# Optimization experiments

Measured on AMD Instinct MI355X. Metric: run time of the kernel, lower is better.

Reference implementation:

```python
import jax, jax.numpy as jnp
import numpy as np

EMB = 64
D = 2 * EMB          # 128, feature dim of R / hidden of attention MLP
B, L = 128, 4096     # batch, sequence length
N_ITER = 50          # bisection iterations (entmax_bisect default)


def entmax_bisect(X, alpha, n_iter=N_ITER):
    """alpha-entmax via bisection over the last axis. X: [B, L], alpha: [B, 1] (>1)."""
    am1 = alpha - 1.0
    Xs = X * am1
    d = X.shape[-1]
    inv = 1.0 / am1
    max_val = jnp.max(Xs, axis=-1, keepdims=True)
    tau_lo0 = max_val - 1.0                       # gp(1, alpha) = 1
    tau_hi = max_val - (1.0 / d) ** am1           # gp(1/d, alpha)

    def p(tau):
        return jnp.clip(Xs - tau, 0.0, None) ** inv

    f_lo = jnp.sum(p(tau_lo0), axis=-1, keepdims=True) - 1.0

    def body(i, carry):
        tau_lo, dm, _ = carry
        dm = dm * 0.5
        tau_m = tau_lo + dm
        f_m = jnp.sum(p(tau_m), axis=-1, keepdims=True) - 1.0
        tau_lo = jnp.where(f_m * f_lo >= 0, tau_m, tau_lo)
        return (tau_lo, dm, tau_m)

    _, _, tau_m = jax.lax.fori_loop(0, n_iter, body, (tau_lo0, tau_hi - tau_lo0, tau_lo0))
    p_m = p(tau_m)
    return p_m / jnp.sum(p_m, axis=-1, keepdims=True)  # ensure_sum_one


def setup_inputs() -> dict:
    key = jax.random.key(0)
    ks = jax.random.split(key, 9)
    s = 1.0 / np.sqrt(D)
    R = jax.random.normal(ks[0], (B, L, D), dtype=jnp.float32)
    alpha = 1.25 + 0.5 * jax.random.uniform(ks[1], (B, 1), dtype=jnp.float32)  # in (1.25, 1.75)
    target = jax.random.normal(ks[2], (B, 1, D), dtype=jnp.float32)
    Wr1 = s * jax.random.normal(ks[3], (D, D), dtype=jnp.float32)      # Linear(2E, 2E), no bias
    Wr2 = s * jax.random.normal(ks[4], (D, EMB), dtype=jnp.float32)    # Linear(E, 2E) (shape-fixed), no bias
    Wr3 = s * jax.random.normal(ks[5], (1, D), dtype=jnp.float32)      # Linear(2E, 1), no bias
    bias_r = s * jax.random.normal(ks[6], (D,), dtype=jnp.float32)
    Wf_w = s * jax.random.normal(ks[7], (EMB, D), dtype=jnp.float32)   # Linear(2E, E)
    Wf_b = s * jax.random.normal(ks[8], (EMB,), dtype=jnp.float32)
    return {"R": R, "alpha": alpha, "target": target, "Wr1": Wr1, "Wr2": Wr2,
            "Wr3": Wr3, "bias_r": bias_r, "Wf_w": Wf_w, "Wf_b": Wf_b}


def reference(R, alpha, target, Wr1, Wr2, Wr3, bias_r, Wf_w, Wf_b):
    # q = Wf(target): [B, 1, E]
    q = jnp.einsum('btd,ed->bte', target, Wf_w) + Wf_b
    # additive attention score: Wr3 @ relu(Wr1 k + Wr2 q + b): [B, L]
    h = jax.nn.relu(jnp.einsum('bld,ed->ble', R, Wr1)
                    + jnp.einsum('bte,de->btd', q, Wr2)
                    + bias_r)
    scores = jnp.einsum('bld,d->bl', h, Wr3[0])
    # entmax sparsification over the sequence axis
    a = entmax_bisect(scores, alpha)
    # weighted sum of v = R: [B, D]
    res = jnp.einsum('bl,bld->bd', a, R)
    res = jax.nn.selu(res)
    res = res / jnp.linalg.norm(res, axis=-1, keepdims=True)
    return res
```

## Files before the change

### kernel.cpp

```cpp
#include <hip/hip_runtime.h>
#include <hip/hip_bf16.h>

#define B_ 128
#define L_ 4096
#define D_ 128
#define E_ 64

typedef __attribute__((ext_vector_type(8))) short short8;
typedef __attribute__((ext_vector_type(4))) float floatx4;

static __device__ __forceinline__ unsigned short f2bf(float x) {
  __hip_bfloat16 h = __float2bfloat16(x);
  union { __hip_bfloat16 h; unsigned short u; } c; c.h = h; return c.u;
}
static __device__ __forceinline__ float bf2f(unsigned short u) {
  union { unsigned short u; __hip_bfloat16 h; } c; c.u = u; return __bfloat162float(c.h);
}

__global__ __launch_bounds__(256) void prep(
    const float* __restrict__ Wr1, unsigned short* __restrict__ hi,
    unsigned short* __restrict__ lo, const float* __restrict__ target,
    const float* __restrict__ Wr2, const float* __restrict__ bias_r,
    const float* __restrict__ Wf_w, const float* __restrict__ Wf_b,
    float* __restrict__ cvec) {
  if (blockIdx.x < 64) {
    int t = blockIdx.x * 256 + threadIdx.x;
    int j = t & 7, lane = (t >> 3) & 63, ks = (t >> 9) & 3, nt = t >> 11;
    int e = nt * 16 + (lane & 15);
    int d = ks * 32 + (lane >> 4) * 8 + j;
    float x = Wr1[e * D_ + d];
    unsigned short h = f2bf(x);
    hi[t] = h;
    lo[t] = f2bf(x - bf2f(h));
  } else {
    const int sub = threadIdx.x >> 7;
    const int t = threadIdx.x & 127;
    const int b = (blockIdx.x - 64) * 2 + sub;
    __shared__ float tg[2][D_];
    __shared__ float q[2][E_];
    tg[sub][t] = target[b * D_ + t];
    __syncthreads();
    if (t < E_) {
      float s = Wf_b[t];
      #pragma unroll 8
      for (int d = 0; d < D_; ++d) s += tg[sub][d] * Wf_w[t * D_ + d];
      q[sub][t] = s;
    }
    __syncthreads();
    float s = bias_r[t];
    #pragma unroll 8
    for (int e = 0; e < E_; ++e) s += q[sub][e] * Wr2[t * E_ + e];
    cvec[b * D_ + t] = s;
  }
}

__global__ __launch_bounds__(256, 2) void pass_b(
    const float* __restrict__ R, const unsigned short* __restrict__ Whi,
    const unsigned short* __restrict__ Wlo, const float* __restrict__ cvec,
    const float* __restrict__ Wr3, float* __restrict__ scores) {
  __shared__ __align__(16) unsigned short sAhi[16384];
  __shared__ __align__(16) unsigned short sAlo[16384];
  const int b = blockIdx.x >> 5;
  const int lt = blockIdx.x & 31;
  const int t = threadIdx.x;
  const int wave = t >> 6, lane = t & 63;
  const int col = lane & 15, quad = lane >> 4;

  const float* Rbase = R + ((size_t)b * L_ + (size_t)lt * 128) * D_;
  #pragma unroll
  for (int i = 0; i < 8; ++i) {
    const int mt = wave * 2 + (i >> 2);
    const int ks = i & 3;
    const int row = mt * 16 + (lane & 15);
    const int c0 = ks * 32 + (lane >> 4) * 8;
    const float4* p = (const float4*)(Rbase + (size_t)row * D_ + c0);
    float4 v0 = p[0], v1 = p[1];
    float vv[8] = {v0.x, v0.y, v0.z, v0.w, v1.x, v1.y, v1.z, v1.w};
    union { unsigned short u[8]; short8 v; } H, Lo;
    #pragma unroll
    for (int j = 0; j < 8; ++j) {
      unsigned short h = f2bf(vv[j]);
      H.u[j] = h;
      Lo.u[j] = f2bf(vv[j] - bf2f(h));
    }
    const int base = ((mt * 4 + ks) * 64 + lane) * 8;
    *(short8*)(sAhi + base) = H.v;
    *(short8*)(sAlo + base) = Lo.v;
  }

  short8 bh[2][4], bl[2][4];
  #pragma unroll
  for (int n = 0; n < 2; ++n)
    #pragma unroll
    for (int ks = 0; ks < 4; ++ks) {
      int off = (((wave * 2 + n) * 4 + ks) * 64 + lane) * 8;
      bh[n][ks] = *(const short8*)(Whi + off);
      bl[n][ks] = *(const short8*)(Wlo + off);
    }

  floatx4 acc[8][2];
  #pragma unroll
  for (int mt = 0; mt < 8; ++mt)
    #pragma unroll
    for (int n = 0; n < 2; ++n) acc[mt][n] = (floatx4){0.f, 0.f, 0.f, 0.f};

  __syncthreads();

  #pragma unroll
  for (int mt = 0; mt < 8; ++mt) {
    #pragma unroll
    for (int ks = 0; ks < 4; ++ks) {
      int ai = ((mt * 4 + ks) * 64 + lane) * 8;
      short8 ah = *(const short8*)(sAhi + ai);
      short8 al = *(const short8*)(sAlo + ai);
      #pragma unroll
      for (int n = 0; n < 2; ++n) {
        acc[mt][n] = __builtin_amdgcn_mfma_f32_16x16x32_bf16(ah, bh[n][ks], acc[mt][n], 0, 0, 0);
        acc[mt][n] = __builtin_amdgcn_mfma_f32_16x16x32_bf16(al, bh[n][ks], acc[mt][n], 0, 0, 0);
        acc[mt][n] = __builtin_amdgcn_mfma_f32_16x16x32_bf16(ah, bl[n][ks], acc[mt][n], 0, 0, 0);
      }
    }
  }

  float w3[2], cb[2];
  #pragma unroll
  for (int n = 0; n < 2; ++n) {
    int e = (wave * 2 + n) * 16 + col;
    w3[n] = Wr3[e];
    cb[n] = cvec[b * D_ + e];
  }
  float part[8][4];
  #pragma unroll
  for (int mt = 0; mt < 8; ++mt)
    #pragma unroll
    for (int r = 0; r < 4; ++r) {
      float s = 0.f;
      #pragma unroll
      for (int n = 0; n < 2; ++n)
        s += w3[n] * fmaxf(acc[mt][n][r] + cb[n], 0.f);
      s += __shfl_xor(s, 1, 64);
      s += __shfl_xor(s, 2, 64);
      s += __shfl_xor(s, 4, 64);
      s += __shfl_xor(s, 8, 64);
      part[mt][r] = s;
    }
  __syncthreads();
  float* red = (float*)sAhi;
  if (col == 0) {
    #pragma unroll
    for (int mt = 0; mt < 8; ++mt)
      #pragma unroll
      for (int r = 0; r < 4; ++r)
        red[wave * 128 + mt * 16 + quad * 4 + r] = part[mt][r];
  }
  __syncthreads();
  if (t < 128) {
    float s = (red[t] + red[128 + t]) + (red[256 + t] + red[384 + t]);
    scores[(size_t)b * L_ + lt * 128 + t] = s;
  }
}

__global__ __launch_bounds__(512) void pass_cd(
    const float* __restrict__ scores, const float* __restrict__ alpha,
    const float* __restrict__ R, float* __restrict__ out) {
  const int b = blockIdx.x, t = threadIdx.x;
  const int wave = t >> 6, lane = t & 63;
  __shared__ float sX[L_];
  __shared__ unsigned short sI[L_];
  __shared__ float sW[L_];
  __shared__ unsigned short sJ[L_];
  __shared__ float ppart[512];
  __shared__ float sred[2][8];
  __shared__ int scnt, smcnt;
  const float am1 = alpha[b] - 1.0f;
  const float inv = 1.0f / am1;
  const float* S = scores + (size_t)b * L_;
  float Xs[8];
  #pragma unroll
  for (int i = 0; i < 8; ++i) Xs[i] = S[i * 512 + t] * am1;
  if (t == 0) { scnt = 0; smcnt = 0; }

  float mx = Xs[0];
  #pragma unroll
  for (int i = 1; i < 8; ++i) mx = fmaxf(mx, Xs[i]);
  #pragma unroll
  for (int m = 32; m >= 1; m >>= 1) mx = fmaxf(mx, __shfl_xor(mx, m, 64));
  if (lane == 0) sred[0][wave] = mx;
  __syncthreads();
  mx = sred[0][0];
  #pragma unroll
  for (int w = 1; w < 8; ++w) mx = fmaxf(mx, sred[0][w]);

  const float tau_lo0 = mx - 1.0f;
  #pragma unroll
  for (int i = 0; i < 8; ++i) {
    if (Xs[i] > tau_lo0) {
      int pos = atomicAdd(&scnt, 1);
      sX[pos] = Xs[i];
      sI[pos] = (unsigned short)(i * 512 + t);
    }
  }
  __syncthreads();
  const int n = scnt;

  float tau_lo = tau_lo0;
  float dm = (mx - exp2f(-12.0f * am1)) - tau_lo;

  int pc = 1;
  auto sumP = [&](float tau) -> float {
    const int par = pc & 1;
    ++pc;
    float s = 0.f;
    for (int k = t; k < n; k += 512) {
      float u = sX[k] - tau;
      if (u > 0.f) s += exp2f(inv * __log2f(u));
    }
    #pragma unroll
    for (int m = 32; m >= 1; m >>= 1) s += __shfl_xor(s, m, 64);
    if (lane == 0) sred[par][wave] = s;
    __syncthreads();
    float r = sred[par][0];
    #pragma unroll
    for (int w = 1; w < 8; ++w) r += sred[par][w];
    return r;
  };

  const float f_lo = sumP(tau_lo) - 1.0f;
  float tau_m = tau_lo;
  for (int it = 0; it < 40; ++it) {
    dm *= 0.5f;
    tau_m = tau_lo + dm;
    float f_m = sumP(tau_m) - 1.0f;
    if (f_m * f_lo >= 0.f) tau_lo = tau_m;
  }

  float s = 0.f;
  for (int k = t; k < n; k += 512) {
    float u = sX[k] - tau_m;
    if (u > 0.f) {
      float p = exp2f(inv * __log2f(u));
      s += p;
      int pos = atomicAdd(&smcnt, 1);
      sJ[pos] = sI[k];
      sW[pos] = p;
    }
  }
  {
    const int par = pc & 1;
    ++pc;
    #pragma unroll
    for (int m = 32; m >= 1; m >>= 1) s += __shfl_xor(s, m, 64);
    if (lane == 0) sred[par][wave] = s;
    __syncthreads();
    s = sred[par][0];
    #pragma unroll
    for (int w = 1; w < 8; ++w) s += sred[par][w];
  }
  const int ns = smcnt;
  const float rs = 1.0f / s;

  const float* Rb = R + (size_t)b * L_ * D_;
  const int g = t >> 7, c = t & 127;
  float acc = 0.f;
  int k = g;
  for (; k + 4 < ns; k += 8) {
    int i0 = sJ[k], i1 = sJ[k + 4];
    float w0 = sW[k], w1 = sW[k + 4];
    acc += w0 * Rb[(size_t)i0 * D_ + c] + w1 * Rb[(size_t)i1 * D_ + c];
  }
  for (; k < ns; k += 4) acc += sW[k] * Rb[(size_t)sJ[k] * D_ + c];
  __syncthreads();
  ppart[t] = acc;
  __syncthreads();
  float r = 0.f;
  if (t < 128) {
    float a2 = ((ppart[t] + ppart[t + 128]) + (ppart[t + 256] + ppart[t + 384])) * rs;
    const float sc = 1.0507009873554805f, al = 1.6732632423543772f;
    r = a2 > 0.f ? sc * a2 : sc * al * (expf(a2) - 1.0f);
  }
  float q = r * r;
  #pragma unroll
  for (int m = 32; m >= 1; m >>= 1) q += __shfl_xor(q, m, 64);
  if (lane == 0) sred[0][wave] = q;
  __syncthreads();
  if (t < 128) {
    float nrm = sqrtf(sred[0][0] + sred[0][1]);
    out[b * D_ + t] = r / nrm;
  }
}

extern "C" void kernel_launch(void* const* d_in, const int* in_sizes, int n_in,
                              void* d_out, int out_size, void* d_ws, size_t ws_size,
                              hipStream_t stream) {
  const float* R      = (const float*)d_in[0];
  const float* alpha  = (const float*)d_in[1];
  const float* target = (const float*)d_in[2];
  const float* Wr1    = (const float*)d_in[3];
  const float* Wr2    = (const float*)d_in[4];
  const float* Wr3    = (const float*)d_in[5];
  const float* bias_r = (const float*)d_in[6];
  const float* Wf_w   = (const float*)d_in[7];
  const float* Wf_b   = (const float*)d_in[8];
  float* out = (float*)d_out;

  char* ws = (char*)d_ws;
  float* cvec          = (float*)ws;
  unsigned short* whi  = (unsigned short*)(ws + 65536);
  unsigned short* wlo  = (unsigned short*)(ws + 98304);
  float* scores        = (float*)(ws + 131072);

  hipLaunchKernelGGL(prep, dim3(128), dim3(256), 0, stream,
                     Wr1, whi, wlo, target, Wr2, bias_r, Wf_w, Wf_b, cvec);
  hipLaunchKernelGGL(pass_b, dim3(B_ * 32), dim3(256), 0, stream,
                     R, whi, wlo, cvec, Wr3, scores);
  hipLaunchKernelGGL(pass_cd, dim3(B_), dim3(512), 0, stream,
                     scores, alpha, R, out);
}
```

Baseline: 468.3 us.

## Remove LDS staging from score GEMM, shrink entmax block, cut bisection iterations

The score kernel now has each wave load and split its own 32 rows of R directly into registers and compute all 128 output columns. This removes the LDS staging buffers, both block barriers and the cross-wave reduction, at the cost of each wave reloading the whole weight matrix. The entmax kernel drops from 512 to 256 threads, which makes its many per-iteration barriers cheaper, and the gather loop is unrolled four-wide. Bisection iterations are cut from 40 to 32, well below the reference's 50, so the threshold precision may drop.

```diff
diff --git a/kernel.cpp b/kernel.cpp
--- a/kernel.cpp
+++ b/kernel.cpp
@@ -54,113 +54,81 @@
   }
 }
 
-__global__ __launch_bounds__(256, 2) void pass_b(
+__global__ __launch_bounds__(256) void pass_b(
     const float* __restrict__ R, const unsigned short* __restrict__ Whi,
     const unsigned short* __restrict__ Wlo, const float* __restrict__ cvec,
     const float* __restrict__ Wr3, float* __restrict__ scores) {
-  __shared__ __align__(16) unsigned short sAhi[16384];
-  __shared__ __align__(16) unsigned short sAlo[16384];
   const int b = blockIdx.x >> 5;
   const int lt = blockIdx.x & 31;
   const int t = threadIdx.x;
   const int wave = t >> 6, lane = t & 63;
   const int col = lane & 15, quad = lane >> 4;
 
-  const float* Rbase = R + ((size_t)b * L_ + (size_t)lt * 128) * D_;
-  #pragma unroll
-  for (int i = 0; i < 8; ++i) {
-    const int mt = wave * 2 + (i >> 2);
-    const int ks = i & 3;
-    const int row = mt * 16 + (lane & 15);
-    const int c0 = ks * 32 + (lane >> 4) * 8;
-    const float4* p = (const float4*)(Rbase + (size_t)row * D_ + c0);
-    float4 v0 = p[0], v1 = p[1];
-    float vv[8] = {v0.x, v0.y, v0.z, v0.w, v1.x, v1.y, v1.z, v1.w};
-    union { unsigned short u[8]; short8 v; } H, Lo;
-    #pragma unroll
-    for (int j = 0; j < 8; ++j) {
-      unsigned short h = f2bf(vv[j]);
-      H.u[j] = h;
-      Lo.u[j] = f2bf(vv[j] - bf2f(h));
-    }
-    const int base = ((mt * 4 + ks) * 64 + lane) * 8;
-    *(short8*)(sAhi + base) = H.v;
-    *(short8*)(sAlo + base) = Lo.v;
-  }
-
-  short8 bh[2][4], bl[2][4];
-  #pragma unroll
-  for (int n = 0; n < 2; ++n)
-    #pragma unroll
-    for (int ks = 0; ks < 4; ++ks) {
-      int off = (((wave * 2 + n) * 4 + ks) * 64 + lane) * 8;
-      bh[n][ks] = *(const short8*)(Whi + off);
-      bl[n][ks] = *(const short8*)(Wlo + off);
-    }
-
-  floatx4 acc[8][2];
-  #pragma unroll
-  for (int mt = 0; mt < 8; ++mt)
-    #pragma unroll
-    for (int n = 0; n < 2; ++n) acc[mt][n] = (floatx4){0.f, 0.f, 0.f, 0.f};
-
-  __syncthreads();
-
-  #pragma unroll
-  for (int mt = 0; mt < 8; ++mt) {
-    #pragma unroll
-    for (int ks = 0; ks < 4; ++ks) {
-      int ai = ((mt * 4 + ks) * 64 + lane) * 8;
-      short8 ah = *(const short8*)(sAhi + ai);
-      short8 al = *(const short8*)(sAlo + ai);
+  const float* Rw = R + ((size_t)b * L_ + (size_t)lt * 128 + wave * 32) * D_;
+
+  floatx4 acc[2][8];
+  #pragma unroll
+  for (int mt = 0; mt < 2; ++mt)
+    #pragma unroll
+    for (int nt = 0; nt < 8; ++nt) acc[mt][nt] = (floatx4){0.f, 0.f, 0.f, 0.f};
+
+  #pragma unroll
+  for (int ks = 0; ks < 4; ++ks) {
+    short8 ah[2], al[2];
+    #pragma unroll
+    for (int mt = 0; mt < 2; ++mt) {
+      const float4* p = (const float4*)(Rw + (size_t)(mt * 16 + col) * D_ + ks * 32 + quad * 8);
+      float4 v0 = p[0], v1 = p[1];
+      float vv[8] = {v0.x, v0.y, v0.z, v0.w, v1.x, v1.y, v1.z, v1.w};
+      union { unsigned short u[8]; short8 v; } H, Lo;
       #pragma unroll
-      for (int n = 0; n < 2; ++n) {
-        acc[mt][n] = __builtin_amdgcn_mfma_f32_16x16x32_bf16(ah, bh[n][ks], acc[mt][n], 0, 0, 0);
-        acc[mt][n] = __builtin_amdgcn_mfma_f32_16x16x32_bf16(al, bh[n][ks], acc[mt][n], 0, 0, 0);
-        acc[mt][n] = __builtin_amdgcn_mfma_f32_16x16x32_bf16(ah, bl[n][ks], acc[mt][n], 0, 0, 0);
+      for (int j = 0; j < 8; ++j) {
+        unsigned short h = f2bf(vv[j]);
+        H.u[j] = h;
+        Lo.u[j] = f2bf(vv[j] - bf2f(h));
       }
-    }
-  }
-
-  float w3[2], cb[2];
-  #pragma unroll
-  for (int n = 0; n < 2; ++n) {
-    int e = (wave * 2 + n) * 16 + col;
-    w3[n] = Wr3[e];
-    cb[n] = cvec[b * D_ + e];
-  }
-  float part[8][4];
-  #pragma unroll
-  for (int mt = 0; mt < 8; ++mt)
+      ah[mt] = H.v;
+      al[mt] = Lo.v;
+    }
+    #pragma unroll
+    for (int nt = 0; nt < 8; ++nt) {
+      const int off = ((nt * 4 + ks) * 64 + lane) * 8;
+      short8 bhv = *(const short8*)(Whi + off);
+      short8 blv = *(const short8*)(Wlo + off);
+      #pragma unroll
+      for (int mt = 0; mt < 2; ++mt) {
+        acc[mt][nt] = __builtin_amdgcn_mfma_f32_16x16x32_bf16(ah[mt], bhv, acc[mt][nt], 0, 0, 0);
+        acc[mt][nt] = __builtin_amdgcn_mfma_f32_16x16x32_bf16(al[mt], bhv, acc[mt][nt], 0, 0, 0);
+        acc[mt][nt] = __builtin_amdgcn_mfma_f32_16x16x32_bf16(ah[mt], blv, acc[mt][nt], 0, 0, 0);
+      }
+    }
+  }
+
+  float w3v[8], cbv[8];
+  #pragma unroll
+  for (int nt = 0; nt < 8; ++nt) {
+    const int e = nt * 16 + col;
+    w3v[nt] = Wr3[e];
+    cbv[nt] = cvec[b * D_ + e];
+  }
+  float* Sout = scores + (size_t)b * L_ + lt * 128 + wave * 32;
+  #pragma unroll
+  for (int mt = 0; mt < 2; ++mt)
     #pragma unroll
     for (int r = 0; r < 4; ++r) {
       float s = 0.f;
       #pragma unroll
-      for (int n = 0; n < 2; ++n)
-        s += w3[n] * fmaxf(acc[mt][n][r] + cb[n], 0.f);
+      for (int nt = 0; nt < 8; ++nt)
+        s += w3v[nt] * fmaxf(acc[mt][nt][r] + cbv[nt], 0.f);
       s += __shfl_xor(s, 1, 64);
       s += __shfl_xor(s, 2, 64);
       s += __shfl_xor(s, 4, 64);
       s += __shfl_xor(s, 8, 64);
-      part[mt][r] = s;
-    }
-  __syncthreads();
-  float* red = (float*)sAhi;
-  if (col == 0) {
-    #pragma unroll
-    for (int mt = 0; mt < 8; ++mt)
-      #pragma unroll
-      for (int r = 0; r < 4; ++r)
-        red[wave * 128 + mt * 16 + quad * 4 + r] = part[mt][r];
-  }
-  __syncthreads();
-  if (t < 128) {
-    float s = (red[t] + red[128 + t]) + (red[256 + t] + red[384 + t]);
-    scores[(size_t)b * L_ + lt * 128 + t] = s;
-  }
-}
-
-__global__ __launch_bounds__(512) void pass_cd(
+      if (col == 0) Sout[mt * 16 + quad * 4 + r] = s;
+    }
+}
+
+__global__ __launch_bounds__(256) void pass_cd(
     const float* __restrict__ scores, const float* __restrict__ alpha,
     const float* __restrict__ R, float* __restrict__ out) {
   const int b = blockIdx.x, t = threadIdx.x;
@@ -169,35 +137,33 @@
   __shared__ unsigned short sI[L_];
   __shared__ float sW[L_];
   __shared__ unsigned short sJ[L_];
-  __shared__ float ppart[512];
-  __shared__ float sred[2][8];
+  __shared__ float ppart[256];
+  __shared__ float sred[2][4];
   __shared__ int scnt, smcnt;
   const float am1 = alpha[b] - 1.0f;
   const float inv = 1.0f / am1;
   const float* S = scores + (size_t)b * L_;
-  float Xs[8];
-  #pragma unroll
-  for (int i = 0; i < 8; ++i) Xs[i] = S[i * 512 + t] * am1;
+  float Xs[16];
+  #pragma unroll
+  for (int i = 0; i < 16; ++i) Xs[i] = S[i * 256 + t] * am1;
   if (t == 0) { scnt = 0; smcnt = 0; }
 
   float mx = Xs[0];
   #pragma unroll
-  for (int i = 1; i < 8; ++i) mx = fmaxf(mx, Xs[i]);
+  for (int i = 1; i < 16; ++i) mx = fmaxf(mx, Xs[i]);
   #pragma unroll
   for (int m = 32; m >= 1; m >>= 1) mx = fmaxf(mx, __shfl_xor(mx, m, 64));
   if (lane == 0) sred[0][wave] = mx;
   __syncthreads();
-  mx = sred[0][0];
-  #pragma unroll
-  for (int w = 1; w < 8; ++w) mx = fmaxf(mx, sred[0][w]);
+  mx = fmaxf(fmaxf(sred[0][0], sred[0][1]), fmaxf(sred[0][2], sred[0][3]));
 
   const float tau_lo0 = mx - 1.0f;
   #pragma unroll
-  for (int i = 0; i < 8; ++i) {
+  for (int i = 0; i < 16; ++i) {
     if (Xs[i] > tau_lo0) {
       int pos = atomicAdd(&scnt, 1);
       sX[pos] = Xs[i];
-      sI[pos] = (unsigned short)(i * 512 + t);
+      sI[pos] = (unsigned short)(i * 256 + t);
     }
   }
   __syncthreads();
@@ -211,7 +177,7 @@
     const int par = pc & 1;
     ++pc;
     float s = 0.f;
-    for (int k = t; k < n; k += 512) {
+    for (int k = t; k < n; k += 256) {
       float u = sX[k] - tau;
       if (u > 0.f) s += exp2f(inv * __log2f(u));
     }
@@ -219,15 +185,12 @@
     for (int m = 32; m >= 1; m >>= 1) s += __shfl_xor(s, m, 64);
     if (lane == 0) sred[par][wave] = s;
     __syncthreads();
-    float r = sred[par][0];
-    #pragma unroll
-    for (int w = 1; w < 8; ++w) r += sred[par][w];
-    return r;
+    return (sred[par][0] + sred[par][1]) + (sred[par][2] + sred[par][3]);
   };
 
   const float f_lo = sumP(tau_lo) - 1.0f;
   float tau_m = tau_lo;
-  for (int it = 0; it < 40; ++it) {
+  for (int it = 0; it < 32; ++it) {
     dm *= 0.5f;
     tau_m = tau_lo + dm;
     float f_m = sumP(tau_m) - 1.0f;
@@ -235,7 +198,7 @@
   }
 
   float s = 0.f;
-  for (int k = t; k < n; k += 512) {
+  for (int k = t; k < n; k += 256) {
     float u = sX[k] - tau_m;
     if (u > 0.f) {
       float p = exp2f(inv * __log2f(u));
@@ -252,36 +215,35 @@
     for (int m = 32; m >= 1; m >>= 1) s += __shfl_xor(s, m, 64);
     if (lane == 0) sred[par][wave] = s;
     __syncthreads();
-    s = sred[par][0];
-    #pragma unroll
-    for (int w = 1; w < 8; ++w) s += sred[par][w];
+    s = (sred[par][0] + sred[par][1]) + (sred[par][2] + sred[par][3]);
   }
   const int ns = smcnt;
   const float rs = 1.0f / s;
 
   const float* Rb = R + (size_t)b * L_ * D_;
   const int g = t >> 7, c = t & 127;
-  float acc = 0.f;
+  float a0 = 0.f;
   int k = g;
-  for (; k + 4 < ns; k += 8) {
-    int i0 = sJ[k], i1 = sJ[k + 4];
-    float w0 = sW[k], w1 = sW[k + 4];
-    acc += w0 * Rb[(size_t)i0 * D_ + c] + w1 * Rb[(size_t)i1 * D_ + c];
-  }
-  for (; k < ns; k += 4) acc += sW[k] * Rb[(size_t)sJ[k] * D_ + c];
-  __syncthreads();
-  ppart[t] = acc;
+  for (; k + 6 < ns; k += 8) {
+    int i0 = sJ[k], i1 = sJ[k + 2], i2 = sJ[k + 4], i3 = sJ[k + 6];
+    float w0 = sW[k], w1 = sW[k + 2], w2 = sW[k + 4], w3v = sW[k + 6];
+    a0 += w0 * Rb[(size_t)i0 * D_ + c] + w1 * Rb[(size_t)i1 * D_ + c]
+        + w2 * Rb[(size_t)i2 * D_ + c] + w3v * Rb[(size_t)i3 * D_ + c];
+  }
+  for (; k < ns; k += 2) a0 += sW[k] * Rb[(size_t)sJ[k] * D_ + c];
+  __syncthreads();
+  ppart[t] = a0;
   __syncthreads();
   float r = 0.f;
   if (t < 128) {
-    float a2 = ((ppart[t] + ppart[t + 128]) + (ppart[t + 256] + ppart[t + 384])) * rs;
+    float a2 = (ppart[t] + ppart[t + 128]) * rs;
     const float sc = 1.0507009873554805f, al = 1.6732632423543772f;
     r = a2 > 0.f ? sc * a2 : sc * al * (expf(a2) - 1.0f);
   }
-  float q = r * r;
-  #pragma unroll
-  for (int m = 32; m >= 1; m >>= 1) q += __shfl_xor(q, m, 64);
-  if (lane == 0) sred[0][wave] = q;
+  float qq = r * r;
+  #pragma unroll
+  for (int m = 32; m >= 1; m >>= 1) qq += __shfl_xor(qq, m, 64);
+  if (lane == 0) sred[0][wave] = qq;
   __syncthreads();
   if (t < 128) {
     float nrm = sqrtf(sred[0][0] + sred[0][1]);
@@ -313,6 +275,6 @@
                      Wr1, whi, wlo, target, Wr2, bias_r, Wf_w, Wf_b, cvec);
   hipLaunchKernelGGL(pass_b, dim3(B_ * 32), dim3(256), 0, stream,
                      R, whi, wlo, cvec, Wr3, scores);
-  hipLaunchKernelGGL(pass_cd, dim3(B_), dim3(512), 0, stream,
+  hipLaunchKernelGGL(pass_cd, dim3(B_), dim3(256), 0, stream,
                      scores, alpha, R, out);
 }
```

Result: slower. 510.5 us (+9.0%).
